# Kernel optimization log

Measured on AMD Instinct MI355X. Metric: run time of the kernel, lower is better.

Reference implementation:

```python
import jax, jax.numpy as jnp
import numpy as np

WEIGHT_THRESH = 0.5
EPS = 1e-5


def setup_inputs() -> dict:
    key = jax.random.key(0)
    k1, k2, k3 = jax.random.split(key, 3)
    B, N = 2048, 4096
    src_points = jax.random.normal(k1, (B, N, 3), dtype=jnp.float32)
    tgt_points = jax.random.normal(k2, (B, N, 3), dtype=jnp.float32)
    weights = jax.random.uniform(k3, (B, N), dtype=jnp.float32)
    return {"src_points": src_points, "tgt_points": tgt_points, "weights": weights}


def reference(src_points, tgt_points, weights):
    # threshold + normalize weights  (B, N)
    w = jnp.where(weights < WEIGHT_THRESH, jnp.zeros_like(weights), weights)
    w = w / (jnp.sum(w, axis=1, keepdims=True) + EPS)
    w = w[:, :, None]  # (B, N, 1)

    # weighted centroids (B, 1, 3)
    src_centroid = jnp.sum(src_points * w, axis=1, keepdims=True)
    ref_centroid = jnp.sum(tgt_points * w, axis=1, keepdims=True)

    src_c = src_points - src_centroid
    ref_c = tgt_points - ref_centroid

    # weighted 3x3 covariance H = src_c^T @ (ref_c * w)   (B, 3, 3)
    H = jnp.einsum('bni,bnj->bij', src_c, ref_c * w)

    # Kabsch: tf.linalg.svd returns S, U, V (V not transposed); jnp returns U, S, Vh
    U, S, Vh = jnp.linalg.svd(H)
    V = jnp.swapaxes(Vh, -1, -2)
    Ut = jnp.swapaxes(U, -1, -2)
    det = jnp.linalg.det(jnp.matmul(V, Ut))  # (B,)

    ones = jnp.ones_like(det)
    d = jnp.stack([ones, ones, jnp.sign(det)], axis=-1)  # (B, 3) diag of sign-fix eye
    R = jnp.matmul(V * d[:, None, :], Ut)  # V @ diag(d) @ U^T  (B, 3, 3)

    t = ref_centroid[:, 0, :] - jnp.einsum('bij,bj->bi', R, src_centroid[:, 0, :])  # (B, 3)
    return R, t
```

## Files before the change

### kernel.cpp

```cpp
#include <hip/hip_runtime.h>
#include <math.h>

#define BATCH   2048
#define NPTS    4096
#define THREADS 256
#define WTHRESH 0.5f
#define EPS     1e-5

__device__ __forceinline__ void accumulate(const float* __restrict__ sb,
                                           const float* __restrict__ tb,
                                           const float* __restrict__ wb,
                                           float* acc) {
  const int t = threadIdx.x;
#pragma unroll
  for (int i = 0; i < 16; ++i) acc[i] = 0.f;

#pragma unroll
  for (int k = 0; k < 4; ++k) {
    const int p0 = (t + k * THREADS) * 4;
    float4 w4 = *(const float4*)(wb + p0);
    const float4* sp = (const float4*)(sb + (size_t)p0 * 3);
    float4 s0 = sp[0], s1 = sp[1], s2 = sp[2];
    const float4* tp = (const float4*)(tb + (size_t)p0 * 3);
    float4 r0 = tp[0], r1 = tp[1], r2 = tp[2];

    float ww[4] = {w4.x, w4.y, w4.z, w4.w};
    float ps[4][3] = {{s0.x, s0.y, s0.z}, {s0.w, s1.x, s1.y},
                      {s1.z, s1.w, s2.x}, {s2.y, s2.z, s2.w}};
    float qs[4][3] = {{r0.x, r0.y, r0.z}, {r0.w, r1.x, r1.y},
                      {r1.z, r1.w, r2.x}, {r2.y, r2.z, r2.w}};
#pragma unroll
    for (int i = 0; i < 4; ++i) {
      float w = (ww[i] < WTHRESH) ? 0.f : ww[i];
      acc[0] += w;
      float wp0 = w * ps[i][0], wp1 = w * ps[i][1], wp2 = w * ps[i][2];
      acc[1] += wp0; acc[2] += wp1; acc[3] += wp2;
      acc[4] += w * qs[i][0]; acc[5] += w * qs[i][1]; acc[6] += w * qs[i][2];
      acc[7]  += wp0 * qs[i][0]; acc[8]  += wp0 * qs[i][1]; acc[9]  += wp0 * qs[i][2];
      acc[10] += wp1 * qs[i][0]; acc[11] += wp1 * qs[i][1]; acc[12] += wp1 * qs[i][2];
      acc[13] += wp2 * qs[i][0]; acc[14] += wp2 * qs[i][1]; acc[15] += wp2 * qs[i][2];
    }
  }
}

__device__ __forceinline__ void reduce_block16(float* acc, float* red ) {
#pragma unroll
  for (int off = 32; off > 0; off >>= 1) {
#pragma unroll
    for (int i = 0; i < 16; ++i) acc[i] += __shfl_down(acc[i], off, 64);
  }
  const int wave = threadIdx.x >> 6;
  const int lane = threadIdx.x & 63;
  if (lane == 0) {
#pragma unroll
    for (int i = 0; i < 16; ++i) red[wave * 16 + i] = acc[i];
  }
  __syncthreads();
  if (threadIdx.x == 0) {
#pragma unroll
    for (int w = 1; w < 4; ++w)
#pragma unroll
      for (int i = 0; i < 16; ++i) acc[i] += red[w * 16 + i];
  }
}

__device__ void solve_from_acc(const float* acc, float* R9, float* t3) {
  double W = acc[0];
  double inv = 1.0 / (W + EPS);
  double sc[3], tc[3];
#pragma unroll
  for (int i = 0; i < 3; ++i) { sc[i] = (double)acc[1 + i] * inv; tc[i] = (double)acc[4 + i] * inv; }
  double ssum = W * inv;

  double H[3][3];
#pragma unroll
  for (int i = 0; i < 3; ++i)
#pragma unroll
    for (int j = 0; j < 3; ++j)
      H[i][j] = (double)acc[7 + 3 * i + j] * inv - sc[i] * tc[j] * (2.0 - ssum);

  double A[3][3];
#pragma unroll
  for (int i = 0; i < 3; ++i)
#pragma unroll
    for (int j = 0; j < 3; ++j)
      A[i][j] = H[0][i] * H[0][j] + H[1][i] * H[1][j] + H[2][i] * H[2][j];

  double V[3][3] = {{1, 0, 0}, {0, 1, 0}, {0, 0, 1}};

  const int PQ[3][2] = {{0, 1}, {0, 2}, {1, 2}};
  for (int sweep = 0; sweep < 15; ++sweep) {
    double off = fabs(A[0][1]) + fabs(A[0][2]) + fabs(A[1][2]);
    if (off < 1e-28) break;
#pragma unroll
    for (int r = 0; r < 3; ++r) {
      int p = PQ[r][0], q = PQ[r][1];
      double apq = A[p][q];
      if (fabs(apq) < 1e-300) continue;
      double theta = (A[q][q] - A[p][p]) / (2.0 * apq);
      double tj = copysign(1.0, theta) / (fabs(theta) + sqrt(theta * theta + 1.0));
      double c = 1.0 / sqrt(tj * tj + 1.0);
      double sn = tj * c;
#pragma unroll
      for (int k = 0; k < 3; ++k) {
        double akp = A[k][p], akq = A[k][q];
        A[k][p] = c * akp - sn * akq;
        A[k][q] = sn * akp + c * akq;
      }
#pragma unroll
      for (int k = 0; k < 3; ++k) {
        double apk = A[p][k], aqk = A[q][k];
        A[p][k] = c * apk - sn * aqk;
        A[q][k] = sn * apk + c * aqk;
      }
#pragma unroll
      for (int k = 0; k < 3; ++k) {
        double vkp = V[k][p], vkq = V[k][q];
        V[k][p] = c * vkp - sn * vkq;
        V[k][q] = sn * vkp + c * vkq;
      }
    }
  }

  double e[3] = {A[0][0], A[1][1], A[2][2]};
  int i0 = 0, i1 = 1, i2 = 2, tswap;
  if (e[i0] < e[i1]) { tswap = i0; i0 = i1; i1 = tswap; }
  if (e[i0] < e[i2]) { tswap = i0; i0 = i2; i2 = tswap; }
  if (e[i1] < e[i2]) { tswap = i1; i1 = i2; i2 = tswap; }

  double v1[3], v2[3], v3[3];
#pragma unroll
  for (int k = 0; k < 3; ++k) { v1[k] = V[k][i0]; v2[k] = V[k][i1]; v3[k] = V[k][i2]; }

  double u1[3], u2[3];
#pragma unroll
  for (int k = 0; k < 3; ++k) u1[k] = H[k][0] * v1[0] + H[k][1] * v1[1] + H[k][2] * v1[2];
  double n1 = sqrt(u1[0] * u1[0] + u1[1] * u1[1] + u1[2] * u1[2]);
  if (n1 > 1e-150) { double r = 1.0 / n1; u1[0] *= r; u1[1] *= r; u1[2] *= r; }
  else { u1[0] = 1.0; u1[1] = 0.0; u1[2] = 0.0; }

#pragma unroll
  for (int k = 0; k < 3; ++k) u2[k] = H[k][0] * v2[0] + H[k][1] * v2[1] + H[k][2] * v2[2];
  double d12 = u1[0] * u2[0] + u1[1] * u2[1] + u1[2] * u2[2];
#pragma unroll
  for (int k = 0; k < 3; ++k) u2[k] -= d12 * u1[k];
  double n2 = sqrt(u2[0] * u2[0] + u2[1] * u2[1] + u2[2] * u2[2]);
  if (n2 > 1e-150) { double r = 1.0 / n2; u2[0] *= r; u2[1] *= r; u2[2] *= r; }
  else {
    double ax = fabs(u1[0]);
    double t0 = (ax < 0.9) ? 1.0 : 0.0, t1v = (ax < 0.9) ? 0.0 : 1.0;
    u2[0] = t0 - (t0 * u1[0] + t1v * u1[1]) * u1[0];
    u2[1] = t1v - (t0 * u1[0] + t1v * u1[1]) * u1[1];
    u2[2] = -(t0 * u1[0] + t1v * u1[1]) * u1[2];
    double nn = sqrt(u2[0] * u2[0] + u2[1] * u2[1] + u2[2] * u2[2]);
    u2[0] /= nn; u2[1] /= nn; u2[2] /= nn;
  }

  double w3[3] = {u1[1] * u2[2] - u1[2] * u2[1],
                  u1[2] * u2[0] - u1[0] * u2[2],
                  u1[0] * u2[1] - u1[1] * u2[0]};

  double cx = v2[1] * v3[2] - v2[2] * v3[1];
  double cy = v2[2] * v3[0] - v2[0] * v3[2];
  double cz = v2[0] * v3[1] - v2[1] * v3[0];
  double detV = v1[0] * cx + v1[1] * cy + v1[2] * cz;
  detV = (detV >= 0.0) ? 1.0 : -1.0;

  double R[3][3];
#pragma unroll
  for (int i = 0; i < 3; ++i)
#pragma unroll
    for (int j = 0; j < 3; ++j)
      R[i][j] = v1[i] * u1[j] + v2[i] * u2[j] + detV * v3[i] * w3[j];

#pragma unroll
  for (int i = 0; i < 3; ++i) {
#pragma unroll
    for (int j = 0; j < 3; ++j) R9[3 * i + j] = (float)R[i][j];
    t3[i] = (float)(tc[i] - (R[i][0] * sc[0] + R[i][1] * sc[1] + R[i][2] * sc[2]));
  }
}

__global__ __launch_bounds__(THREADS) void wp_reduce(const float* __restrict__ src,
                                                     const float* __restrict__ tgt,
                                                     const float* __restrict__ wts,
                                                     float* __restrict__ partials) {
  __shared__ float red[64];
  const int b = blockIdx.x;
  float acc[16];
  accumulate(src + (size_t)b * NPTS * 3, tgt + (size_t)b * NPTS * 3,
             wts + (size_t)b * NPTS, acc);
  reduce_block16(acc, red);
  if (threadIdx.x == 0) {
#pragma unroll
    for (int i = 0; i < 16; ++i) partials[b * 16 + i] = acc[i];
  }
}

__global__ void wp_solve(const float* __restrict__ partials, float* __restrict__ out) {
  const int b = blockIdx.x * blockDim.x + threadIdx.x;
  if (b >= BATCH) return;
  float acc[16];
#pragma unroll
  for (int i = 0; i < 16; ++i) acc[i] = partials[b * 16 + i];
  float R9[9], t3[3];
  solve_from_acc(acc, R9, t3);
#pragma unroll
  for (int i = 0; i < 9; ++i) out[(size_t)b * 9 + i] = R9[i];
#pragma unroll
  for (int i = 0; i < 3; ++i) out[(size_t)BATCH * 9 + (size_t)b * 3 + i] = t3[i];
}

__global__ __launch_bounds__(THREADS) void wp_fused(const float* __restrict__ src,
                                                    const float* __restrict__ tgt,
                                                    const float* __restrict__ wts,
                                                    float* __restrict__ out) {
  __shared__ float red[64];
  const int b = blockIdx.x;
  float acc[16];
  accumulate(src + (size_t)b * NPTS * 3, tgt + (size_t)b * NPTS * 3,
             wts + (size_t)b * NPTS, acc);
  reduce_block16(acc, red);
  if (threadIdx.x == 0) {
    float R9[9], t3[3];
    solve_from_acc(acc, R9, t3);
#pragma unroll
    for (int i = 0; i < 9; ++i) out[(size_t)b * 9 + i] = R9[i];
#pragma unroll
    for (int i = 0; i < 3; ++i) out[(size_t)BATCH * 9 + (size_t)b * 3 + i] = t3[i];
  }
}

extern "C" void kernel_launch(void* const* d_in, const int* in_sizes, int n_in,
                              void* d_out, int out_size, void* d_ws, size_t ws_size,
                              hipStream_t stream) {
  const float* src = (const float*)d_in[0];
  const float* tgt = (const float*)d_in[1];
  const float* wts = (const float*)d_in[2];
  float* out = (float*)d_out;

  if (ws_size >= (size_t)BATCH * 16 * sizeof(float)) {
    float* partials = (float*)d_ws;
    wp_reduce<<<BATCH, THREADS, 0, stream>>>(src, tgt, wts, partials);
    wp_solve<<<(BATCH + 255) / 256, 256, 0, stream>>>(partials, out);
  } else {
    wp_fused<<<BATCH, THREADS, 0, stream>>>(src, tgt, wts, out);
  }
}
```

Before: 247.4 us.

## Split per-batch reduction across four blocks and spread solve over more blocks

```diff
diff --git a/kernel.cpp b/kernel.cpp
--- a/kernel.cpp
+++ b/kernel.cpp
@@ -4,42 +4,39 @@
 #define BATCH   2048
 #define NPTS    4096
 #define THREADS 256
+#define CHUNKS  4
+#define CPTS    (NPTS / CHUNKS)
 #define WTHRESH 0.5f
 #define EPS     1e-5
 
-__device__ __forceinline__ void accumulate(const float* __restrict__ sb,
-                                           const float* __restrict__ tb,
-                                           const float* __restrict__ wb,
-                                           float* acc) {
-  const int t = threadIdx.x;
+__device__ __forceinline__ void accumulate4(const float* __restrict__ sb,
+                                            const float* __restrict__ tb,
+                                            const float* __restrict__ wb,
+                                            float* acc) {
+  const int p0 = threadIdx.x * 4;
+  float4 w4 = *(const float4*)(wb + p0);
+  const float4* sp = (const float4*)(sb + (size_t)p0 * 3);
+  float4 s0 = sp[0], s1 = sp[1], s2 = sp[2];
+  const float4* tp = (const float4*)(tb + (size_t)p0 * 3);
+  float4 r0 = tp[0], r1 = tp[1], r2 = tp[2];
+
+  float ww[4] = {w4.x, w4.y, w4.z, w4.w};
+  float ps[4][3] = {{s0.x, s0.y, s0.z}, {s0.w, s1.x, s1.y},
+                    {s1.z, s1.w, s2.x}, {s2.y, s2.z, s2.w}};
+  float qs[4][3] = {{r0.x, r0.y, r0.z}, {r0.w, r1.x, r1.y},
+                    {r1.z, r1.w, r2.x}, {r2.y, r2.z, r2.w}};
 #pragma unroll
   for (int i = 0; i < 16; ++i) acc[i] = 0.f;
-
-#pragma unroll
-  for (int k = 0; k < 4; ++k) {
-    const int p0 = (t + k * THREADS) * 4;
-    float4 w4 = *(const float4*)(wb + p0);
-    const float4* sp = (const float4*)(sb + (size_t)p0 * 3);
-    float4 s0 = sp[0], s1 = sp[1], s2 = sp[2];
-    const float4* tp = (const float4*)(tb + (size_t)p0 * 3);
-    float4 r0 = tp[0], r1 = tp[1], r2 = tp[2];
-
-    float ww[4] = {w4.x, w4.y, w4.z, w4.w};
-    float ps[4][3] = {{s0.x, s0.y, s0.z}, {s0.w, s1.x, s1.y},
-                      {s1.z, s1.w, s2.x}, {s2.y, s2.z, s2.w}};
-    float qs[4][3] = {{r0.x, r0.y, r0.z}, {r0.w, r1.x, r1.y},
-                      {r1.z, r1.w, r2.x}, {r2.y, r2.z, r2.w}};
-#pragma unroll
-    for (int i = 0; i < 4; ++i) {
-      float w = (ww[i] < WTHRESH) ? 0.f : ww[i];
-      acc[0] += w;
-      float wp0 = w * ps[i][0], wp1 = w * ps[i][1], wp2 = w * ps[i][2];
-      acc[1] += wp0; acc[2] += wp1; acc[3] += wp2;
-      acc[4] += w * qs[i][0]; acc[5] += w * qs[i][1]; acc[6] += w * qs[i][2];
-      acc[7]  += wp0 * qs[i][0]; acc[8]  += wp0 * qs[i][1]; acc[9]  += wp0 * qs[i][2];
-      acc[10] += wp1 * qs[i][0]; acc[11] += wp1 * qs[i][1]; acc[12] += wp1 * qs[i][2];
-      acc[13] += wp2 * qs[i][0]; acc[14] += wp2 * qs[i][1]; acc[15] += wp2 * qs[i][2];
-    }
+#pragma unroll
+  for (int i = 0; i < 4; ++i) {
+    float w = (ww[i] < WTHRESH) ? 0.f : ww[i];
+    acc[0] += w;
+    float wp0 = w * ps[i][0], wp1 = w * ps[i][1], wp2 = w * ps[i][2];
+    acc[1] += wp0; acc[2] += wp1; acc[3] += wp2;
+    acc[4] += w * qs[i][0]; acc[5] += w * qs[i][1]; acc[6] += w * qs[i][2];
+    acc[7]  += wp0 * qs[i][0]; acc[8]  += wp0 * qs[i][1]; acc[9]  += wp0 * qs[i][2];
+    acc[10] += wp1 * qs[i][0]; acc[11] += wp1 * qs[i][1]; acc[12] += wp1 * qs[i][2];
+    acc[13] += wp2 * qs[i][0]; acc[14] += wp2 * qs[i][1]; acc[15] += wp2 * qs[i][2];
   }
 }
 
@@ -89,9 +86,9 @@
   double V[3][3] = {{1, 0, 0}, {0, 1, 0}, {0, 0, 1}};
 
   const int PQ[3][2] = {{0, 1}, {0, 2}, {1, 2}};
-  for (int sweep = 0; sweep < 15; ++sweep) {
+  for (int sweep = 0; sweep < 8; ++sweep) {
     double off = fabs(A[0][1]) + fabs(A[0][2]) + fabs(A[1][2]);
-    if (off < 1e-28) break;
+    if (off < 1e-26) break;
 #pragma unroll
     for (int r = 0; r < 3; ++r) {
       int p = PQ[r][0], q = PQ[r][1];
@@ -181,28 +178,36 @@
   }
 }
 
-__global__ __launch_bounds__(THREADS) void wp_reduce(const float* __restrict__ src,
-                                                     const float* __restrict__ tgt,
-                                                     const float* __restrict__ wts,
-                                                     float* __restrict__ partials) {
+__global__ __launch_bounds__(THREADS) void wp_reduce_split(const float* __restrict__ src,
+                                                           const float* __restrict__ tgt,
+                                                           const float* __restrict__ wts,
+                                                           float* __restrict__ partials) {
   __shared__ float red[64];
-  const int b = blockIdx.x;
+  const int bid = blockIdx.x;
+  const int b = bid >> 2;
+  const int c = bid & 3;
+  const size_t off = (size_t)b * NPTS + (size_t)c * CPTS;
   float acc[16];
-  accumulate(src + (size_t)b * NPTS * 3, tgt + (size_t)b * NPTS * 3,
-             wts + (size_t)b * NPTS, acc);
+  accumulate4(src + off * 3, tgt + off * 3, wts + off, acc);
   reduce_block16(acc, red);
   if (threadIdx.x == 0) {
 #pragma unroll
-    for (int i = 0; i < 16; ++i) partials[b * 16 + i] = acc[i];
-  }
-}
-
-__global__ void wp_solve(const float* __restrict__ partials, float* __restrict__ out) {
-  const int b = blockIdx.x * blockDim.x + threadIdx.x;
+    for (int i = 0; i < 16; ++i) partials[(size_t)bid * 16 + i] = acc[i];
+  }
+}
+
+__global__ __launch_bounds__(64) void wp_solve(const float* __restrict__ partials,
+                                               float* __restrict__ out) {
+  const int b = blockIdx.x * 64 + threadIdx.x;
   if (b >= BATCH) return;
   float acc[16];
 #pragma unroll
-  for (int i = 0; i < 16; ++i) acc[i] = partials[b * 16 + i];
+  for (int i = 0; i < 16; ++i) acc[i] = 0.f;
+#pragma unroll
+  for (int cch = 0; cch < CHUNKS; ++cch)
+#pragma unroll
+    for (int i = 0; i < 16; ++i)
+      acc[i] += partials[(size_t)(b * CHUNKS + cch) * 16 + i];
   float R9[9], t3[3];
   solve_from_acc(acc, R9, t3);
 #pragma unroll
@@ -217,9 +222,16 @@
                                                     float* __restrict__ out) {
   __shared__ float red[64];
   const int b = blockIdx.x;
+  float accT[16];
   float acc[16];
-  accumulate(src + (size_t)b * NPTS * 3, tgt + (size_t)b * NPTS * 3,
-             wts + (size_t)b * NPTS, acc);
+#pragma unroll
+  for (int i = 0; i < 16; ++i) acc[i] = 0.f;
+  for (int c = 0; c < CHUNKS; ++c) {
+    const size_t off = (size_t)b * NPTS + (size_t)c * CPTS;
+    accumulate4(src + off * 3, tgt + off * 3, wts + off, accT);
+#pragma unroll
+    for (int i = 0; i < 16; ++i) acc[i] += accT[i];
+  }
   reduce_block16(acc, red);
   if (threadIdx.x == 0) {
     float R9[9], t3[3];
@@ -239,10 +251,10 @@
   const float* wts = (const float*)d_in[2];
   float* out = (float*)d_out;
 
-  if (ws_size >= (size_t)BATCH * 16 * sizeof(float)) {
+  if (ws_size >= (size_t)BATCH * CHUNKS * 16 * sizeof(float)) {
     float* partials = (float*)d_ws;
-    wp_reduce<<<BATCH, THREADS, 0, stream>>>(src, tgt, wts, partials);
-    wp_solve<<<(BATCH + 255) / 256, 256, 0, stream>>>(partials, out);
+    wp_reduce_split<<<BATCH * CHUNKS, THREADS, 0, stream>>>(src, tgt, wts, partials);
+    wp_solve<<<(BATCH + 63) / 64, 64, 0, stream>>>(partials, out);
   } else {
     wp_fused<<<BATCH, THREADS, 0, stream>>>(src, tgt, wts, out);
   }
```

Result: no change. 243.6 us (-1.5%).
